# Optimization experiments

Measured on AMD Instinct MI355X. Metric: run time of the kernel, lower is better.

Reference implementation:

```python
import jax, jax.numpy as jnp
import numpy as np

VOL_RES = 128          # volume_res
SIGMA = 0.05           # gaussian splat sigma (normalized [0,1] coords)
SPLAT_R = 3            # splat neighborhood radius = smooth_kernel_size // 2
TET_W = 5              # tet rasterization window edge (voxels)
EPS_W = 1e-3           # weight_sum init (torch fills 0.001)

B, NV, NSURF, NF, NT = 2, 7700, 6890, 13776, 30000


def setup_inputs() -> dict:
    key = jax.random.key(0)
    k0, k1, k2, k3 = jax.random.split(key, 4)
    smpl_vertices = jax.random.uniform(k0, (B, NV, 3), dtype=jnp.float32)      # verts in [0,1]^3
    vertex_code = jax.random.uniform(k1, (B, NSURF, 3), dtype=jnp.float32)     # semantic code per surface vert
    face_indices = jax.random.randint(k2, (NF, 3), 0, NSURF, dtype=jnp.int32)
    tet_indices = jax.random.randint(k3, (NT, 4), 0, NV, dtype=jnp.int32)
    return {"smpl_vertices": smpl_vertices, "vertex_code": vertex_code,
            "face_indices": face_indices, "tet_indices": tet_indices}


def _voxelize(smpl_vertices, vertex_code, face_indices, tet_indices):
    R = VOL_RES
    R3 = R * R * R
    bsz = smpl_vertices.shape[0]

    # --- face centers / normals (computed by the torch forward; not consumed by the kernel) ---
    faces = smpl_vertices[:, face_indices]                         # (B,NF,3,3)
    face_center = faces.mean(axis=2)                               # (B,NF,3)
    v10 = faces[:, :, 0] - faces[:, :, 1]
    v12 = faces[:, :, 2] - faces[:, :, 1]
    nrm = jnp.cross(v10, v12)
    face_normal = nrm / jnp.maximum(
        jnp.linalg.norm(nrm, axis=-1, keepdims=True), 1e-5)        # F.normalize eps=1e-5
    del face_center, face_normal  # passed to the autograd fn but unused by the cuda op

    bidx = jnp.arange(bsz, dtype=jnp.int32)

    # ---------------- occupancy from tetrahedrons (point-in-tet rasterization) ----------------
    tets = smpl_vertices[:, tet_indices]                           # (B,NT,4,3)
    a = tets[:, :, 0]
    e1 = tets[:, :, 1] - a
    e2 = tets[:, :, 2] - a
    e3 = tets[:, :, 3] - a
    c23 = jnp.cross(e2, e3)
    vol6 = jnp.sum(e1 * c23, axis=-1)                              # signed 6*volume (B,NT)

    anchor = jnp.floor(jnp.min(tets, axis=2) * R).astype(jnp.int32)  # (B,NT,3) min-corner voxel
    w1 = jnp.arange(TET_W, dtype=jnp.int32)
    toff = jnp.stack(jnp.meshgrid(w1, w1, w1, indexing="ij"), -1).reshape(-1, 3)  # (W3,3) xyz
    tvox = anchor[:, :, None, :] + toff                            # (B,NT,W3,3)
    tp = (tvox.astype(jnp.float32) + 0.5) / R                      # voxel centers
    p = tp - a[:, :, None, :]                                      # (B,NT,W3,3)
    iv = 1.0 / jnp.where(jnp.abs(vol6) > 1e-12, vol6, 1.0)
    l1 = jnp.sum(p * c23[:, :, None, :], -1) * iv[:, :, None]
    l2 = jnp.sum(jnp.cross(p, e3[:, :, None, :]) * e1[:, :, None, :], -1) * iv[:, :, None]
    l3 = jnp.sum(jnp.cross(e2[:, :, None, :], p) * e1[:, :, None, :], -1) * iv[:, :, None]
    inside = (l1 >= 0) & (l2 >= 0) & (l3 >= 0) & (l1 + l2 + l3 <= 1.0)
    inside &= (jnp.abs(vol6) > 1e-12)[:, :, None]
    tvalid = jnp.all((tvox >= 0) & (tvox < R), axis=-1) & inside   # (B,NT,W3)
    # linear index, layout (b, z, y, x)
    tlin = ((bidx[:, None, None] * R + tvox[..., 2]) * R + tvox[..., 1]) * R + tvox[..., 0]
    tlin = jnp.where(tvalid, tlin, bsz * R3)                       # drop out-of-range
    occ = jnp.zeros((bsz * R3,), jnp.float32).at[tlin.reshape(-1)].max(
        tvalid.astype(jnp.float32).reshape(-1), mode="drop")

    # ---------------- gaussian semantic splat from surface vertices ----------------
    vs = smpl_vertices[:, :NSURF]                                  # (B,NS,3)
    base = jnp.floor(vs * R).astype(jnp.int32)                     # containing voxel
    o1 = jnp.arange(-SPLAT_R, SPLAT_R + 1, dtype=jnp.int32)
    offs = jnp.stack(jnp.meshgrid(o1, o1, o1, indexing="ij"), -1).reshape(-1, 3)  # (K3,3)
    svox = base[:, :, None, :] + offs                              # (B,NS,K3,3)
    ctr = (svox.astype(jnp.float32) + 0.5) / R
    d2 = jnp.sum((ctr - vs[:, :, None, :]) ** 2, axis=-1)          # (B,NS,K3)
    w = jnp.exp(-d2 / (2.0 * SIGMA * SIGMA))
    svalid = jnp.all((svox >= 0) & (svox < R), axis=-1)
    w = jnp.where(svalid, w, 0.0)
    slin = ((bidx[:, None, None] * R + svox[..., 2]) * R + svox[..., 1]) * R + svox[..., 0]
    slin = jnp.where(svalid, slin, bsz * R3).reshape(-1)

    wsum = jnp.full((bsz * R3,), EPS_W, jnp.float32).at[slin].add(w.reshape(-1), mode="drop")
    contrib = (w[..., None] * vertex_code[:, :, None, :]).reshape(-1, 3)
    sem = jnp.zeros((bsz * R3, 3), jnp.float32).at[slin].add(contrib, mode="drop")

    semantic = sem / wsum[:, None] * occ[:, None]                  # normalize + mask to body
    semantic = semantic.reshape(bsz, R, R, R, 3)                   # (B, z, y, x, C)
    return jnp.transpose(semantic, (0, 4, 1, 2, 3))                # (B, C, z, y, x)


def reference(smpl_vertices, vertex_code, face_indices, tet_indices):
    return _voxelize(smpl_vertices, vertex_code, face_indices, tet_indices)
```

## Files before the change

kernel.cpp:

```cpp
#include <hip/hip_runtime.h>
#include <math.h>

#define R 128
#define R3 (R*R*R)
#define BATCH 2
#define NV 7700
#define NSURF 6890
#define NT 30000
#define EPS_W 0.001f

#define NC 32
#define NCELLS (BATCH*NC*NC*NC)
#define CAP 12
#define SLOT_F 8
#define MAXV 256

#define TET_STRIDE 20

__global__ void bin_kernel(const float* __restrict__ verts,
                           const float* __restrict__ code,
                           int*   __restrict__ counts,
                           float* __restrict__ bins) {
    int idx = blockIdx.x * blockDim.x + threadIdx.x;
    if (idx >= BATCH * NSURF) return;
    int v = idx % NSURF;
    int b = idx / NSURF;

    const float* vp = verts + ((size_t)b * NV + v) * 3;
    float px = vp[0], py = vp[1], pz = vp[2];
    int bx = (int)floorf(px * 128.0f);
    int by = (int)floorf(py * 128.0f);
    int bz = (int)floorf(pz * 128.0f);
    bx = min(max(bx, 0), 127); by = min(max(by, 0), 127); bz = min(max(bz, 0), 127);

    int cell = ((b * NC + (bz >> 2)) * NC + (by >> 2)) * NC + (bx >> 2);
    int slot = atomicAdd(counts + cell, 1);
    if (slot < CAP) {
        const float* cp = code + ((size_t)b * NSURF + v) * 3;
        float* s = bins + ((size_t)cell * CAP + slot) * SLOT_F;
        s[0] = px; s[1] = py; s[2] = pz;
        s[3] = cp[0]; s[4] = cp[1]; s[5] = cp[2];
    }
}

__global__ void tet_prep_kernel(const float* __restrict__ verts,
                                const int*   __restrict__ tets,
                                float* __restrict__ td) {
    int bt = blockIdx.x * blockDim.x + threadIdx.x;
    if (bt >= BATCH * NT) return;
    int t = bt % NT;
    int b = bt / NT;

    int4 ti = *(const int4*)(tets + (size_t)t * 4);
    const float* vb = verts + (size_t)b * NV * 3;

    float ax = vb[ti.x*3+0], ay = vb[ti.x*3+1], az = vb[ti.x*3+2];
    float bx = vb[ti.y*3+0], by = vb[ti.y*3+1], bz = vb[ti.y*3+2];
    float cx = vb[ti.z*3+0], cy = vb[ti.z*3+1], cz = vb[ti.z*3+2];
    float dx = vb[ti.w*3+0], dy = vb[ti.w*3+1], dz = vb[ti.w*3+2];

    float e1x = bx-ax, e1y = by-ay, e1z = bz-az;
    float e2x = cx-ax, e2y = cy-ay, e2z = cz-az;
    float e3x = dx-ax, e3y = dy-ay, e3z = dz-az;

    float c23x = e2y*e3z - e2z*e3y;
    float c23y = e2z*e3x - e2x*e3z;
    float c23z = e2x*e3y - e2y*e3x;
    float vol6 = e1x*c23x + e1y*c23y + e1z*c23z;

    int anx  = (int)floorf(fminf(fminf(ax,bx), fminf(cx,dx)) * 128.0f);
    int any_ = (int)floorf(fminf(fminf(ay,by), fminf(cy,dy)) * 128.0f);
    int anz  = (int)floorf(fminf(fminf(az,bz), fminf(cz,dz)) * 128.0f);
    int pk = (anx & 0xFF) | ((any_ & 0xFF) << 8) | ((anz & 0xFF) << 16);

    float* o = td + (size_t)bt * TET_STRIDE;
    float4* o4 = (float4*)o;
    o4[0] = make_float4(ax, ay, az, e1x);
    o4[1] = make_float4(e1y, e1z, e2x, e2y);
    o4[2] = make_float4(e2z, e3x, e3y, e3z);
    o4[3] = make_float4(c23x, c23y, c23z, vol6);
    o4[4] = make_float4(__int_as_float(pk), 0.0f, 0.0f, 0.0f);
}

__global__ void tet_kernel(const float* __restrict__ td,
                           unsigned char* __restrict__ occ) {
    const int total = BATCH * NT * 25;
    int idx = blockIdx.x * blockDim.x + threadIdx.x;
    if (idx >= total) return;
    int k  = idx % 25;
    int bt = idx / 25;
    int b  = bt / NT;

    const float4* o4 = (const float4*)(td + (size_t)bt * TET_STRIDE);
    float4 r0 = o4[0], r1 = o4[1], r2 = o4[2], r3 = o4[3], r4 = o4[4];
    float ax = r0.x, ay = r0.y, az = r0.z;
    float e1x = r0.w, e1y = r1.x, e1z = r1.y;
    float e2x = r1.z, e2y = r1.w, e2z = r2.x;
    float e3x = r2.y, e3y = r2.z, e3z = r2.w;
    float c23x = r3.x, c23y = r3.y, c23z = r3.z;
    float vol6 = r3.w;
    if (fabsf(vol6) <= 1e-12f) return;

    int pk = __float_as_int(r4.x);
    int anx = pk & 0xFF, any_ = (pk >> 8) & 0xFF, anz = (pk >> 16) & 0xFF;

    int vy = any_ + k / 5;
    int vz = anz  + k % 5;
    if ((unsigned)vy >= 128u || (unsigned)vz >= 128u) return;

    const float inv = 1.0f / 128.0f;
    float iv = 1.0f / vol6;
    float py = ((float)vy + 0.5f) * inv - ay;
    float pz = ((float)vz + 0.5f) * inv - az;

    unsigned char* orow = occ + (size_t)b * R3 + ((size_t)vz * R + vy) * R;

    #pragma unroll
    for (int ddx = 0; ddx < 5; ddx++) {
        int vx = anx + ddx;
        if ((unsigned)vx >= 128u) continue;
        float px = ((float)vx + 0.5f) * inv - ax;

        float l1 = (px*c23x + py*c23y + pz*c23z) * iv;
        float cpx = py*e3z - pz*e3y;
        float cpy = pz*e3x - px*e3z;
        float cpz = px*e3y - py*e3x;
        float l2 = (cpx*e1x + cpy*e1y + cpz*e1z) * iv;
        float cqx = e2y*pz - e2z*py;
        float cqy = e2z*px - e2x*pz;
        float cqz = e2x*py - e2y*px;
        float l3 = (cqx*e1x + cqy*e1y + cqz*e1z) * iv;

        if (l1 >= 0.0f && l2 >= 0.0f && l3 >= 0.0f && (l1 + l2 + l3) <= 1.0f)
            orow[vx] = 1;
    }
}

__global__ __launch_bounds__(256) void gather_tile_kernel(
        const unsigned char* __restrict__ occ,
        const int*   __restrict__ counts,
        const float* __restrict__ bins,
        float* __restrict__ out) {
    __shared__ float4 s_a[MAXV];
    __shared__ float4 s_b[MAXV];
    __shared__ int s_n;

    int blk = blockIdx.x;
    int tx = blk & 15, ty = (blk >> 4) & 15, tz = (blk >> 8) & 15, b = blk >> 12;
    int x0 = tx << 3, y0 = ty << 3, z0 = tz << 3;

    if (threadIdx.x == 0) s_n = 0;
    __syncthreads();

    int cx0 = max(x0 - 3, 0) >> 2, cx1 = min(x0 + 10, 127) >> 2;
    int cy0 = max(y0 - 3, 0) >> 2, cy1 = min(y0 + 10, 127) >> 2;
    int cz0 = max(z0 - 3, 0) >> 2, cz1 = min(z0 + 10, 127) >> 2;
    int ncx = cx1 - cx0 + 1, ncy = cy1 - cy0 + 1, ncz = cz1 - cz0 + 1;
    int ncell = ncx * ncy * ncz;

    int t = threadIdx.x;
    if (t < ncell) {
        int lx = t % ncx; int rem = t / ncx;
        int ly = rem % ncy; int lz = rem / ncy;
        int cell = ((b * NC + cz0 + lz) * NC + cy0 + ly) * NC + cx0 + lx;
        int n = min(counts[cell], CAP);
        if (n > 0) {
            int base = atomicAdd(&s_n, n);
            const float* sp = bins + (size_t)cell * CAP * SLOT_F;
            for (int j = 0; j < n; j++, sp += SLOT_F) {
                int d = base + j;
                if (d < MAXV) {
                    float4 A = *(const float4*)sp;
                    float2 Bc = *(const float2*)(sp + 4);
                    int bx = (int)floorf(A.x * 128.0f);
                    int by = (int)floorf(A.y * 128.0f);
                    int bz = (int)floorf(A.z * 128.0f);
                    int pk = bx | (by << 8) | (bz << 16);
                    s_a[d] = A;
                    s_b[d] = make_float4(Bc.x, Bc.y, __int_as_float(pk), 0.0f);
                }
            }
        }
    }
    __syncthreads();
    int nv = min(s_n, MAXV);

    int x = x0 + (t & 7);
    int y = y0 + ((t >> 3) & 7);
    int z = z0 + (t >> 6);

    int L0 = (z * R + y) * R + x;
    int L1 = L0 + 4 * R * R;
    unsigned char o0 = occ[(size_t)b * R3 + L0];
    unsigned char o1 = occ[(size_t)b * R3 + L1];

    float w0 = EPS_W, p0 = 0.0f, q0 = 0.0f, r0 = 0.0f;
    float w1 = EPS_W, p1 = 0.0f, q1 = 0.0f, r1 = 0.0f;

    if (__ballot(o0 | o1)) {
        const float inv = 1.0f / 128.0f;
        float fx  = ((float)x + 0.5f) * inv;
        float fy  = ((float)y + 0.5f) * inv;
        float fz0 = ((float)z + 0.5f) * inv;
        float fz1 = fz0 + 4.0f * inv;
        for (int j = 0; j < nv; j++) {
            float4 A  = s_a[j];
            float4 Bv = s_b[j];
            int pk = __float_as_int(Bv.z);
            int bx = pk & 0xFF, by = (pk >> 8) & 0xFF, bz = (pk >> 16) & 0xFF;
            if (abs(x - bx) <= 3 && abs(y - by) <= 3) {
                float ddx = fx - A.x, ddy = fy - A.y;
                float dxy = ddx*ddx + ddy*ddy;
                int dz0 = z - bz;
                if (abs(dz0) <= 3) {
                    float dd = fz0 - A.z;
                    float w = __expf(-200.0f * (dxy + dd*dd));
                    w0 += w; p0 += w*A.w; q0 += w*Bv.x; r0 += w*Bv.y;
                }
                if (abs(dz0 + 4) <= 3) {
                    float dd = fz1 - A.z;
                    float w = __expf(-200.0f * (dxy + dd*dd));
                    w1 += w; p1 += w*A.w; q1 += w*Bv.x; r1 += w*Bv.y;
                }
            }
        }
    }
    float s0 = o0 ? 1.0f / w0 : 0.0f;
    float s1 = o1 ? 1.0f / w1 : 0.0f;
    float* ob = out + (size_t)b * 3 * R3;
    ob[L0]        = p0 * s0; ob[R3 + L0]   = q0 * s0; ob[2*R3 + L0] = r0 * s0;
    ob[L1]        = p1 * s1; ob[R3 + L1]   = q1 * s1; ob[2*R3 + L1] = r1 * s1;
}

extern "C" void kernel_launch(void* const* d_in, const int* in_sizes, int n_in,
                              void* d_out, int out_size, void* d_ws, size_t ws_size,
                              hipStream_t stream) {
    const float* smpl_vertices = (const float*)d_in[0];
    const float* vertex_code   = (const float*)d_in[1];
    const int*   tet_indices   = (const int*)d_in[3];
    float* out = (float*)d_out;

    unsigned char* occ = (unsigned char*)d_ws;
    int*   counts = (int*)(occ + (size_t)BATCH * R3);
    float* bins   = (float*)(counts + NCELLS);
    float* td     = bins + (size_t)NCELLS * CAP * SLOT_F;

    hipMemsetAsync(occ, 0, (size_t)BATCH * R3 + (size_t)NCELLS * sizeof(int), stream);

    const int bin_total = BATCH * NSURF;
    bin_kernel<<<(bin_total + 255) / 256, 256, 0, stream>>>(smpl_vertices, vertex_code, counts, bins);

    const int nt_total = BATCH * NT;
    tet_prep_kernel<<<(nt_total + 255) / 256, 256, 0, stream>>>(smpl_vertices, tet_indices, td);

    const int tet_total = BATCH * NT * 25;
    tet_kernel<<<(tet_total + 255) / 256, 256, 0, stream>>>(td, occ);

    const int ntiles = BATCH * 16 * 16 * 16;
    gather_tile_kernel<<<ntiles, 256, 0, stream>>>(occ, counts, bins, out);
}
```

Measured before the change: 115.0 us.

## Fuse prep kernels, prefilter splat sources per tile, pair voxels along x

```diff
diff --git a/kernel.cpp b/kernel.cpp
--- a/kernel.cpp
+++ b/kernel.cpp
@@ -13,41 +13,43 @@
 #define NCELLS (BATCH*NC*NC*NC)
 #define CAP 12
 #define SLOT_F 8
-#define MAXV 256
+#define MAXV 128
 
 #define TET_STRIDE 20
-
-__global__ void bin_kernel(const float* __restrict__ verts,
-                           const float* __restrict__ code,
-                           int*   __restrict__ counts,
-                           float* __restrict__ bins) {
+#define BIN_TOTAL (BATCH*NSURF)
+#define NT_TOTAL  (BATCH*NT)
+
+__global__ void prep_kernel(const float* __restrict__ verts,
+                            const float* __restrict__ code,
+                            const int*   __restrict__ tets,
+                            int*   __restrict__ counts,
+                            float* __restrict__ bins,
+                            float* __restrict__ td) {
     int idx = blockIdx.x * blockDim.x + threadIdx.x;
-    if (idx >= BATCH * NSURF) return;
-    int v = idx % NSURF;
-    int b = idx / NSURF;
-
-    const float* vp = verts + ((size_t)b * NV + v) * 3;
-    float px = vp[0], py = vp[1], pz = vp[2];
-    int bx = (int)floorf(px * 128.0f);
-    int by = (int)floorf(py * 128.0f);
-    int bz = (int)floorf(pz * 128.0f);
-    bx = min(max(bx, 0), 127); by = min(max(by, 0), 127); bz = min(max(bz, 0), 127);
-
-    int cell = ((b * NC + (bz >> 2)) * NC + (by >> 2)) * NC + (bx >> 2);
-    int slot = atomicAdd(counts + cell, 1);
-    if (slot < CAP) {
-        const float* cp = code + ((size_t)b * NSURF + v) * 3;
-        float* s = bins + ((size_t)cell * CAP + slot) * SLOT_F;
-        s[0] = px; s[1] = py; s[2] = pz;
-        s[3] = cp[0]; s[4] = cp[1]; s[5] = cp[2];
-    }
-}
-
-__global__ void tet_prep_kernel(const float* __restrict__ verts,
-                                const int*   __restrict__ tets,
-                                float* __restrict__ td) {
-    int bt = blockIdx.x * blockDim.x + threadIdx.x;
-    if (bt >= BATCH * NT) return;
+
+    if (idx < BIN_TOTAL) {
+        int v = idx % NSURF;
+        int b = idx / NSURF;
+        const float* vp = verts + ((size_t)b * NV + v) * 3;
+        float px = vp[0], py = vp[1], pz = vp[2];
+        int bx = (int)floorf(px * 128.0f);
+        int by = (int)floorf(py * 128.0f);
+        int bz = (int)floorf(pz * 128.0f);
+        bx = min(max(bx, 0), 127); by = min(max(by, 0), 127); bz = min(max(bz, 0), 127);
+
+        int cell = ((b * NC + (bz >> 2)) * NC + (by >> 2)) * NC + (bx >> 2);
+        int slot = atomicAdd(counts + cell, 1);
+        if (slot < CAP) {
+            const float* cp = code + ((size_t)b * NSURF + v) * 3;
+            float* s = bins + ((size_t)cell * CAP + slot) * SLOT_F;
+            s[0] = px; s[1] = py; s[2] = pz;
+            s[3] = cp[0]; s[4] = cp[1]; s[5] = cp[2];
+        }
+        return;
+    }
+
+    int bt = idx - BIN_TOTAL;
+    if (bt >= NT_TOTAL) return;
     int t = bt % NT;
     int b = bt / NT;
 
@@ -73,8 +75,7 @@
     int anz  = (int)floorf(fminf(fminf(az,bz), fminf(cz,dz)) * 128.0f);
     int pk = (anx & 0xFF) | ((any_ & 0xFF) << 8) | ((anz & 0xFF) << 16);
 
-    float* o = td + (size_t)bt * TET_STRIDE;
-    float4* o4 = (float4*)o;
+    float4* o4 = (float4*)(td + (size_t)bt * TET_STRIDE);
     o4[0] = make_float4(ax, ay, az, e1x);
     o4[1] = make_float4(e1y, e1z, e2x, e2y);
     o4[2] = make_float4(e2z, e3x, e3y, e3z);
@@ -84,7 +85,7 @@
 
 __global__ void tet_kernel(const float* __restrict__ td,
                            unsigned char* __restrict__ occ) {
-    const int total = BATCH * NT * 25;
+    const int total = NT_TOTAL * 25;
     int idx = blockIdx.x * blockDim.x + threadIdx.x;
     if (idx >= total) return;
     int k  = idx % 25;
@@ -164,17 +165,18 @@
         int ly = rem % ncy; int lz = rem / ncy;
         int cell = ((b * NC + cz0 + lz) * NC + cy0 + ly) * NC + cx0 + lx;
         int n = min(counts[cell], CAP);
-        if (n > 0) {
-            int base = atomicAdd(&s_n, n);
-            const float* sp = bins + (size_t)cell * CAP * SLOT_F;
-            for (int j = 0; j < n; j++, sp += SLOT_F) {
-                int d = base + j;
+        const float* sp = bins + (size_t)cell * CAP * SLOT_F;
+        for (int j = 0; j < n; j++, sp += SLOT_F) {
+            float4 A = *(const float4*)sp;
+            int bx = (int)floorf(A.x * 128.0f);
+            int by = (int)floorf(A.y * 128.0f);
+            int bz = (int)floorf(A.z * 128.0f);
+            if ((unsigned)(bx - x0 + 3) <= 13u &&
+                (unsigned)(by - y0 + 3) <= 13u &&
+                (unsigned)(bz - z0 + 3) <= 13u) {
+                int d = atomicAdd(&s_n, 1);
                 if (d < MAXV) {
-                    float4 A = *(const float4*)sp;
                     float2 Bc = *(const float2*)(sp + 4);
-                    int bx = (int)floorf(A.x * 128.0f);
-                    int by = (int)floorf(A.y * 128.0f);
-                    int bz = (int)floorf(A.z * 128.0f);
                     int pk = bx | (by << 8) | (bz << 16);
                     s_a[d] = A;
                     s_b[d] = make_float4(Bc.x, Bc.y, __int_as_float(pk), 0.0f);
@@ -185,41 +187,40 @@
     __syncthreads();
     int nv = min(s_n, MAXV);
 
-    int x = x0 + (t & 7);
-    int y = y0 + ((t >> 3) & 7);
-    int z = z0 + (t >> 6);
+    int x = x0 + ((t & 3) << 1);
+    int y = y0 + ((t >> 2) & 7);
+    int z = z0 + (t >> 5);
 
     int L0 = (z * R + y) * R + x;
-    int L1 = L0 + 4 * R * R;
-    unsigned char o0 = occ[(size_t)b * R3 + L0];
-    unsigned char o1 = occ[(size_t)b * R3 + L1];
+    unsigned short oc = *(const unsigned short*)(occ + (size_t)b * R3 + L0);
+    int o0 = oc & 0xFF, o1 = oc >> 8;
 
     float w0 = EPS_W, p0 = 0.0f, q0 = 0.0f, r0 = 0.0f;
     float w1 = EPS_W, p1 = 0.0f, q1 = 0.0f, r1 = 0.0f;
 
-    if (__ballot(o0 | o1)) {
+    if (__ballot(oc)) {
         const float inv = 1.0f / 128.0f;
-        float fx  = ((float)x + 0.5f) * inv;
+        float fx0 = ((float)x + 0.5f) * inv;
+        float fx1 = fx0 + inv;
         float fy  = ((float)y + 0.5f) * inv;
-        float fz0 = ((float)z + 0.5f) * inv;
-        float fz1 = fz0 + 4.0f * inv;
+        float fz  = ((float)z + 0.5f) * inv;
         for (int j = 0; j < nv; j++) {
             float4 A  = s_a[j];
             float4 Bv = s_b[j];
             int pk = __float_as_int(Bv.z);
             int bx = pk & 0xFF, by = (pk >> 8) & 0xFF, bz = (pk >> 16) & 0xFF;
-            if (abs(x - bx) <= 3 && abs(y - by) <= 3) {
-                float ddx = fx - A.x, ddy = fy - A.y;
-                float dxy = ddx*ddx + ddy*ddy;
-                int dz0 = z - bz;
-                if (abs(dz0) <= 3) {
-                    float dd = fz0 - A.z;
-                    float w = __expf(-200.0f * (dxy + dd*dd));
+            if ((unsigned)(y - by + 3) <= 6u && (unsigned)(z - bz + 3) <= 6u) {
+                float ddy = fy - A.y, ddz = fz - A.z;
+                float dyz = ddy*ddy + ddz*ddz;
+                int dx0 = x - bx;
+                if ((unsigned)(dx0 + 3) <= 6u) {
+                    float ddx = fx0 - A.x;
+                    float w = __expf(-200.0f * (ddx*ddx + dyz));
                     w0 += w; p0 += w*A.w; q0 += w*Bv.x; r0 += w*Bv.y;
                 }
-                if (abs(dz0 + 4) <= 3) {
-                    float dd = fz1 - A.z;
-                    float w = __expf(-200.0f * (dxy + dd*dd));
+                if ((unsigned)(dx0 + 4) <= 6u) {
+                    float ddx = fx1 - A.x;
+                    float w = __expf(-200.0f * (ddx*ddx + dyz));
                     w1 += w; p1 += w*A.w; q1 += w*Bv.x; r1 += w*Bv.y;
                 }
             }
@@ -227,9 +228,10 @@
     }
     float s0 = o0 ? 1.0f / w0 : 0.0f;
     float s1 = o1 ? 1.0f / w1 : 0.0f;
-    float* ob = out + (size_t)b * 3 * R3;
-    ob[L0]        = p0 * s0; ob[R3 + L0]   = q0 * s0; ob[2*R3 + L0] = r0 * s0;
-    ob[L1]        = p1 * s1; ob[R3 + L1]   = q1 * s1; ob[2*R3 + L1] = r1 * s1;
+    float* ob = out + (size_t)b * 3 * R3 + L0;
+    *(float2*)(ob)        = make_float2(p0 * s0, p1 * s1);
+    *(float2*)(ob + R3)   = make_float2(q0 * s0, q1 * s1);
+    *(float2*)(ob + 2*R3) = make_float2(r0 * s0, r1 * s1);
 }
 
 extern "C" void kernel_launch(void* const* d_in, const int* in_sizes, int n_in,
@@ -247,13 +249,11 @@
 
     hipMemsetAsync(occ, 0, (size_t)BATCH * R3 + (size_t)NCELLS * sizeof(int), stream);
 
-    const int bin_total = BATCH * NSURF;
-    bin_kernel<<<(bin_total + 255) / 256, 256, 0, stream>>>(smpl_vertices, vertex_code, counts, bins);
-
-    const int nt_total = BATCH * NT;
-    tet_prep_kernel<<<(nt_total + 255) / 256, 256, 0, stream>>>(smpl_vertices, tet_indices, td);
-
-    const int tet_total = BATCH * NT * 25;
+    const int prep_total = BIN_TOTAL + NT_TOTAL;
+    prep_kernel<<<(prep_total + 255) / 256, 256, 0, stream>>>(
+        smpl_vertices, vertex_code, tet_indices, counts, bins, td);
+
+    const int tet_total = NT_TOTAL * 25;
     tet_kernel<<<(tet_total + 255) / 256, 256, 0, stream>>>(td, occ);
 
     const int ntiles = BATCH * 16 * 16 * 16;
```

Result: no change. 113.4 us (-1.4%).
